# Optimization experiments

Measured on AMD Instinct MI355X. Metric: run time of the kernel, lower is better.

The kernel has to match this reference:

```python
import jax, jax.numpy as jnp
import numpy as np

EPS = 1e-5

def _layernorm(x, g, b):
    mu = jnp.mean(x, axis=-1, keepdims=True)
    var = jnp.mean(jnp.square(x - mu), axis=-1, keepdims=True)
    return (x - mu) * jax.lax.rsqrt(var + EPS) * g + b

def _mlp(x, w1, b1, w2, b2):
    h = jax.nn.gelu(jnp.einsum('bnd,dh->bnh', x, w1) + b1, approximate=False)
    return jnp.einsum('bnh,hd->bnd', h, w2) + b2

def setup_inputs() -> dict:
    key = jax.random.key(0)
    B, N, D, H = 2, 8192, 1024, 4096
    ks = jax.random.split(key, 12)
    s1 = 1.0 / np.sqrt(D)
    s2 = 1.0 / np.sqrt(H)
    return {
        'x': jax.random.normal(ks[0], (B, N, D), dtype=jnp.float32),
        'mask': jax.random.randint(ks[1], (B, N), 0, 2) > 0,
        'g_rgb': jnp.ones((D,), jnp.float32),
        'b_rgb': jnp.zeros((D,), jnp.float32),
        'w1_rgb': jax.random.normal(ks[2], (D, H), dtype=jnp.float32) * s1,
        'b1_rgb': jnp.zeros((H,), jnp.float32),
        'w2_rgb': jax.random.normal(ks[3], (H, D), dtype=jnp.float32) * s2,
        'b2_rgb': jnp.zeros((D,), jnp.float32),
        'g_expr': jnp.ones((D,), jnp.float32),
        'b_expr': jnp.zeros((D,), jnp.float32),
        'w1_expr': jax.random.normal(ks[4], (D, H), dtype=jnp.float32) * s1,
        'b1_expr': jnp.zeros((H,), jnp.float32),
        'w2_expr': jax.random.normal(ks[5], (H, D), dtype=jnp.float32) * s2,
        'b2_expr': jnp.zeros((D,), jnp.float32),
    }

def reference(x, mask, g_rgb, b_rgb, w1_rgb, b1_rgb, w2_rgb, b2_rgb,
              g_expr, b_expr, w1_expr, b1_expr, w2_expr, b2_expr):
    # Per-token routing: rgb expert where mask, expr expert where ~mask.
    # LayerNorm+MLP are pointwise per token, so dense compute + select is
    # mathematically identical to the torch gather->compute->scatter.
    z_rgb = _mlp(_layernorm(x, g_rgb, b_rgb), w1_rgb, b1_rgb, w2_rgb, b2_rgb)
    z_expr = _mlp(_layernorm(x, g_expr, b_expr), w1_expr, b1_expr, w2_expr, b2_expr)
    z = jnp.where(mask[..., None], z_rgb, z_expr)
    return z.astype(jnp.float16)  # torch scatters into a float16 buffer
```

## Files before the change

### kernel.cpp

```cpp
#include <hip/hip_runtime.h>
#include <hip/hip_bf16.h>
#include <hip/hip_fp16.h>

#define D_ 1024
#define H_ 4096
#define NTOK 16384
#define MPAD 16640

typedef __attribute__((ext_vector_type(8))) short bf16x8;
typedef __attribute__((ext_vector_type(4))) float f32x4;

static __device__ __forceinline__ unsigned short f2bf(float f) {
  union { float f; unsigned u; } x; x.f = f;
  unsigned u = x.u + 0x7fffu + ((x.u >> 16) & 1u);
  return (unsigned short)(u >> 16);
}

static __device__ __forceinline__ void gld16(const void* g, void* l) {
  __builtin_amdgcn_global_load_lds(
      (const __attribute__((address_space(1))) unsigned int*)g,
      (__attribute__((address_space(3))) unsigned int*)l, 16, 0, 0);
}

static __device__ __forceinline__ float gelu_fast(float x) {
  const float z = x * (1.5957691216f + 0.0713548163f * x * x);
  return x * __builtin_amdgcn_rcpf(1.0f + __expf(-z));
}

__global__ __launch_bounds__(256) void transpose4_kernel(
    const float* __restrict__ w1r, const float* __restrict__ w1e,
    const float* __restrict__ w2r, const float* __restrict__ w2e,
    unsigned short* __restrict__ o1r, unsigned short* __restrict__ o1e,
    unsigned short* __restrict__ o2r, unsigned short* __restrict__ o2e) {
  __shared__ float tile[64][65];
  const int t = blockIdx.x;
  const float* src; unsigned short* dst; int R, C, tl;
  if (t < 1024)       { src = w1r; dst = o1r; R = D_; C = H_; tl = t; }
  else if (t < 2048)  { src = w1e; dst = o1e; R = D_; C = H_; tl = t - 1024; }
  else if (t < 3072)  { src = w2r; dst = o2r; R = H_; C = D_; tl = t - 2048; }
  else                { src = w2e; dst = o2e; R = H_; C = D_; tl = t - 3072; }
  const int tc = C >> 6;
  const int r0 = (tl / tc) * 64, c0 = (tl % tc) * 64;
  const int tx = threadIdx.x & 63, ty = threadIdx.x >> 6;
#pragma unroll
  for (int i = 0; i < 64; i += 4)
    tile[ty + i][tx] = src[(size_t)(r0 + ty + i) * C + c0 + tx];
  __syncthreads();
  const int wl = threadIdx.x & 31, wrow = threadIdx.x >> 5;
#pragma unroll
  for (int i = 0; i < 64; i += 8) {
    const int orow = wrow + i;
    const unsigned lo = f2bf(tile[2 * wl][orow]);
    const unsigned hi = f2bf(tile[2 * wl + 1][orow]);
    *(unsigned*)(dst + (size_t)(c0 + orow) * R + r0 + 2 * wl) = lo | (hi << 16);
  }
}

__global__ __launch_bounds__(256) void compact_kernel(
    const int* __restrict__ mask, int* __restrict__ perm, int* __restrict__ counts) {
  const int NT = 256, CH = NTOK / NT;
  __shared__ int sm[NTOK];
  __shared__ int wsum[4];
  const int t = threadIdx.x;
  const int ln = t & 63, wv = t >> 6;
  for (int i = t; i < NTOK; i += NT) sm[i] = mask[i];
  for (int i = t; i < MPAD; i += NT) perm[i] = -1;
  __syncthreads();
  const int base = t * CH;
  int cnt = 0;
  for (int i = 0; i < CH; ++i) cnt += (sm[base + i] != 0);
  int sc = cnt;
#pragma unroll
  for (int o = 1; o < 64; o <<= 1) {
    int u = __shfl_up(sc, o, 64);
    if (ln >= o) sc += u;
  }
  if (ln == 63) wsum[wv] = sc;
  __syncthreads();
  int woff = 0;
#pragma unroll
  for (int j = 0; j < 4; ++j) woff += (j < wv) ? wsum[j] : 0;
  const int total1 = wsum[0] + wsum[1] + wsum[2] + wsum[3];
  if (t == 0) { counts[0] = total1; counts[1] = NTOK - total1; }
  const int excl = woff + sc - cnt;
  const int expr_base = ((total1 + 255) >> 8) << 8;
  int p1 = excl;
  int p0 = expr_base + (base - excl);
  for (int i = 0; i < CH; ++i) {
    const int idx = base + i;
    if (sm[idx] != 0) perm[p1++] = idx; else perm[p0++] = idx;
  }
}

__global__ __launch_bounds__(512) void ln_kernel(
    const float* __restrict__ x, const int* __restrict__ mask,
    const int* __restrict__ perm,
    const float* __restrict__ g_rgb, const float* __restrict__ b_rgb,
    const float* __restrict__ g_expr, const float* __restrict__ b_expr,
    unsigned short* __restrict__ xln) {
  const int h = threadIdx.x >> 8;
  const int tid = threadIdx.x & 255;
  const int i = blockIdx.x * 2 + h;
  int t = perm[i];
  const bool live = t >= 0;
  if (!live) t = 0;
  const float4 v = ((const float4*)(x + (size_t)t * D_))[tid];
  float s = v.x + v.y + v.z + v.w;
  float ss = v.x * v.x + v.y * v.y + v.z * v.z + v.w * v.w;
#pragma unroll
  for (int o = 32; o > 0; o >>= 1) {
    s += __shfl_xor(s, o, 64);
    ss += __shfl_xor(ss, o, 64);
  }
  __shared__ float red[16];
  const int wv = threadIdx.x >> 6, ln = threadIdx.x & 63;
  if (ln == 0) { red[wv] = s; red[8 + wv] = ss; }
  __syncthreads();
  const int rb = h * 4;
  s = red[rb + 0] + red[rb + 1] + red[rb + 2] + red[rb + 3];
  ss = red[8 + rb + 0] + red[8 + rb + 1] + red[8 + rb + 2] + red[8 + rb + 3];
  const float mu = s * (1.0f / D_);
  const float var = ss * (1.0f / D_) - mu * mu;
  const float rs = rsqrtf(var + 1e-5f);
  const bool rgb = mask[t] != 0;
  const float4 gv = ((const float4*)(rgb ? g_rgb : g_expr))[tid];
  const float4 bv = ((const float4*)(rgb ? b_rgb : b_expr))[tid];
  const unsigned short o0 = f2bf((v.x - mu) * rs * gv.x + bv.x);
  const unsigned short o1 = f2bf((v.y - mu) * rs * gv.y + bv.y);
  const unsigned short o2 = f2bf((v.z - mu) * rs * gv.z + bv.z);
  const unsigned short o3 = f2bf((v.w - mu) * rs * gv.w + bv.w);
  uint2 pk;
  pk.x = (unsigned)o0 | ((unsigned)o1 << 16);
  pk.y = (unsigned)o2 | ((unsigned)o3 << 16);
  if (live) *((uint2*)(xln + (size_t)i * D_ + tid * 4)) = pk;
}

template <int K, int N>
__global__ __launch_bounds__(512, 2) void gemm8_kernel(
    const unsigned short* __restrict__ A,
    const unsigned short* __restrict__ Wt_rgb,
    const unsigned short* __restrict__ Wt_expr,
    const float* __restrict__ bias_rgb,
    const float* __restrict__ bias_expr,
    const int* __restrict__ counts,
    unsigned short* __restrict__ Out) {
  constexpr int MT = MPAD / 256;
  constexpr int NT = N / 256;
  constexpr int ntk = K / 64;
  constexpr int KH2 = 128 * K * 2;

  const int tid = threadIdx.x;
  const int id = blockIdx.x;
  const int xcd = id & 7;
  const int slot = id >> 3;
  const int p = xcd * ((MT * NT) / 8) + slot;
  const int m0 = (p / NT) * 256;
  const int n0 = (p % NT) * 256;
  const int cnt_rgb = counts[0];
  const unsigned short* Wt = (m0 < cnt_rgb) ? Wt_rgb : Wt_expr;
  const float* bias = (m0 < cnt_rgb) ? bias_rgb : bias_expr;

  __shared__ unsigned short As[2][256 * 64];
  __shared__ unsigned short Bs[2][256 * 64];

  const int lane = tid & 63, wave = tid >> 6;
  const int wr = wave >> 2, wc = wave & 3;
  const int quad = lane >> 4, l16 = lane & 15;

  f32x4 acc[8][4] = {};

  const char* Abase = (const char*)A;
  const char* Wbase = (const char*)Wt;

  int agK0, agK1, bgK0, bgK1, sl0, sl1;
  {
    const int s0 = tid, s1 = 512 + tid;
    const int r0 = s0 >> 3, r1 = s1 >> 3;
    const int ks0 = ((s0 ^ r0) & 7) * 8, ks1 = ((s1 ^ r1) & 7) * 8;
    agK0 = ((m0 + r0) * K + ks0) * 2;  agK1 = ((m0 + r1) * K + ks1) * 2;
    bgK0 = ((n0 + r0) * K + ks0) * 2;  bgK1 = ((n0 + r1) * K + ks1) * 2;
    sl0 = s0 * 16;  sl1 = s1 * 16;
  }

  int aoffL[2][2][4];
  int boffL[2][4];
#pragma unroll
  for (int kk = 0; kk < 2; ++kk) {
    const int cb = kk * 4 + quad;
#pragma unroll
    for (int mh = 0; mh < 2; ++mh)
#pragma unroll
      for (int mi = 0; mi < 4; ++mi) {
        const int row = wr * 128 + mh * 64 + mi * 16 + l16;
        aoffL[kk][mh][mi] = (row * 64 + ((cb ^ row) & 7) * 8) * 2;
      }
#pragma unroll
    for (int ni = 0; ni < 4; ++ni) {
      const int row = wc * 64 + ni * 16 + l16;
      boffL[kk][ni] = (row * 64 + ((cb ^ row) & 7) * 8) * 2;
    }
  }

  bf16x8 a0, a1, a2, a3;
  bf16x8 bb[4];

#define STAGE_A(T1, HA, Q) do { \
    gld16(Abase + agK0 + (HA) * KH2 + (T1) * 128, (char*)As + (Q) * 32768 + (HA) * 16384 + sl0); \
    gld16(Abase + agK1 + (HA) * KH2 + (T1) * 128, (char*)As + (Q) * 32768 + (HA) * 16384 + sl1); \
  } while (0)
#define STAGE_B(T2, HB, Q) do { \
    gld16(Wbase + bgK0 + (HB) * KH2 + (T2) * 128, (char*)Bs + (Q) * 32768 + (HB) * 16384 + sl0); \
    gld16(Wbase + bgK1 + (HB) * KH2 + (T2) * 128, (char*)Bs + (Q) * 32768 + (HB) * 16384 + sl1); \
  } while (0)
#define RD_A(P_, KK, MH) do { \
    const char* _ab = (const char*)As + (P_) * 32768; \
    a0 = *(const bf16x8*)(_ab + aoffL[KK][MH][0]); \
    a1 = *(const bf16x8*)(_ab + aoffL[KK][MH][1]); \
    a2 = *(const bf16x8*)(_ab + aoffL[KK][MH][2]); \
    a3 = *(const bf16x8*)(_ab + aoffL[KK][MH][3]); \
  } while (0)
#define RD_B(P_, KK) do { \
    const char* _bp = (const char*)Bs + (P_) * 32768; \
    bb[0] = *(const bf16x8*)(_bp + boffL[KK][0]); \
    bb[1] = *(const bf16x8*)(_bp + boffL[KK][1]); \
    bb[2] = *(const bf16x8*)(_bp + boffL[KK][2]); \
    bb[3] = *(const bf16x8*)(_bp + boffL[KK][3]); \
  } while (0)
#define MFMA16(MO) do { \
    acc[(MO)+0][0] = __builtin_amdgcn_mfma_f32_16x16x32_bf16(a0, bb[0], acc[(MO)+0][0], 0, 0, 0); \
    acc[(MO)+0][1] = __builtin_amdgcn_mfma_f32_16x16x32_bf16(a0, bb[1], acc[(MO)+0][1], 0, 0, 0); \
    acc[(MO)+0][2] = __builtin_amdgcn_mfma_f32_16x16x32_bf16(a0, bb[2], acc[(MO)+0][2], 0, 0, 0); \
    acc[(MO)+0][3] = __builtin_amdgcn_mfma_f32_16x16x32_bf16(a0, bb[3], acc[(MO)+0][3], 0, 0, 0); \
    acc[(MO)+1][0] = __builtin_amdgcn_mfma_f32_16x16x32_bf16(a1, bb[0], acc[(MO)+1][0], 0, 0, 0); \
    acc[(MO)+1][1] = __builtin_amdgcn_mfma_f32_16x16x32_bf16(a1, bb[1], acc[(MO)+1][1], 0, 0, 0); \
    acc[(MO)+1][2] = __builtin_amdgcn_mfma_f32_16x16x32_bf16(a1, bb[2], acc[(MO)+1][2], 0, 0, 0); \
    acc[(MO)+1][3] = __builtin_amdgcn_mfma_f32_16x16x32_bf16(a1, bb[3], acc[(MO)+1][3], 0, 0, 0); \
    acc[(MO)+2][0] = __builtin_amdgcn_mfma_f32_16x16x32_bf16(a2, bb[0], acc[(MO)+2][0], 0, 0, 0); \
    acc[(MO)+2][1] = __builtin_amdgcn_mfma_f32_16x16x32_bf16(a2, bb[1], acc[(MO)+2][1], 0, 0, 0); \
    acc[(MO)+2][2] = __builtin_amdgcn_mfma_f32_16x16x32_bf16(a2, bb[2], acc[(MO)+2][2], 0, 0, 0); \
    acc[(MO)+2][3] = __builtin_amdgcn_mfma_f32_16x16x32_bf16(a2, bb[3], acc[(MO)+2][3], 0, 0, 0); \
    acc[(MO)+3][0] = __builtin_amdgcn_mfma_f32_16x16x32_bf16(a3, bb[0], acc[(MO)+3][0], 0, 0, 0); \
    acc[(MO)+3][1] = __builtin_amdgcn_mfma_f32_16x16x32_bf16(a3, bb[1], acc[(MO)+3][1], 0, 0, 0); \
    acc[(MO)+3][2] = __builtin_amdgcn_mfma_f32_16x16x32_bf16(a3, bb[2], acc[(MO)+3][2], 0, 0, 0); \
    acc[(MO)+3][3] = __builtin_amdgcn_mfma_f32_16x16x32_bf16(a3, bb[3], acc[(MO)+3][3], 0, 0, 0); \
  } while (0)

#define KTILE(T_, P_, SA_, SB_, VMC_) do { \
     \
    RD_B(P_, 0); RD_A(P_, 0, 0); \
    if (SA_) STAGE_A((T_) + 1, 0, (P_) ^ 1); \
    __builtin_amdgcn_s_barrier(); \
    __builtin_amdgcn_s_setprio(1); MFMA16(0); __builtin_amdgcn_s_setprio(0); \
    __builtin_amdgcn_s_barrier(); \
     \
    RD_A(P_, 0, 1); \
    if (SA_) STAGE_A((T_) + 1, 1, (P_) ^ 1); \
    __builtin_amdgcn_s_barrier(); \
    __builtin_amdgcn_s_setprio(1); MFMA16(4); __builtin_amdgcn_s_setprio(0); \
    __builtin_amdgcn_s_barrier(); \
     \
    RD_B(P_, 1); RD_A(P_, 1, 0); \
    __builtin_amdgcn_s_barrier(); \
    __builtin_amdgcn_s_setprio(1); MFMA16(0); __builtin_amdgcn_s_setprio(0); \
    __builtin_amdgcn_s_barrier(); \
     \
    RD_A(P_, 1, 1); \
    if (SB_) { STAGE_B((T_) + 2, 0, P_); STAGE_B((T_) + 2, 1, P_); } \
    __builtin_amdgcn_s_barrier(); \
    __builtin_amdgcn_s_setprio(1); MFMA16(4); __builtin_amdgcn_s_setprio(0); \
    if ((VMC_) == 4) { asm volatile("s_waitcnt vmcnt(4)" ::: "memory"); } \
    else if ((VMC_) == 0) { asm volatile("s_waitcnt vmcnt(0)" ::: "memory"); } \
    __builtin_amdgcn_sched_barrier(0); \
    __builtin_amdgcn_s_barrier(); \
  } while (0)

  STAGE_A(0, 0, 0); STAGE_A(0, 1, 0);
  STAGE_B(0, 0, 0); STAGE_B(0, 1, 0);
  STAGE_B(1, 0, 1); STAGE_B(1, 1, 1);
  asm volatile("s_waitcnt vmcnt(4)" ::: "memory");
  __builtin_amdgcn_sched_barrier(0);
  __builtin_amdgcn_s_barrier();

  for (int tt = 0; tt < ntk / 2 - 1; ++tt) {
    const int t0 = tt * 2;
    KTILE(t0, 0, 1, 1, 4);
    KTILE(t0 + 1, 1, 1, 1, 4);
  }
  KTILE(ntk - 2, 0, 1, 0, 0);
  KTILE(ntk - 1, 1, 0, 0, -1);

#undef KTILE
#undef MFMA16
#undef RD_B
#undef RD_A
#undef STAGE_B
#undef STAGE_A

  float bv[4];
#pragma unroll
  for (int ni = 0; ni < 4; ++ni) bv[ni] = bias[n0 + wc * 64 + ni * 16 + l16];
#pragma unroll
  for (int mi = 0; mi < 8; ++mi) {
#pragma unroll
    for (int r = 0; r < 4; ++r) {
      const int row = m0 + wr * 128 + mi * 16 + quad * 4 + r;
      unsigned short* orow = Out + (size_t)row * N + n0 + wc * 64 + l16;
#pragma unroll
      for (int ni = 0; ni < 4; ++ni)
        orow[ni * 16] = f2bf(gelu_fast(acc[mi][ni][r] + bv[ni]));
    }
  }
}

template <int EP, int K, int N>
__global__ __launch_bounds__(256) void gemm_kernel(
    const unsigned short* __restrict__ A,
    const unsigned short* __restrict__ Wt_rgb,
    const unsigned short* __restrict__ Wt_expr,
    const float* __restrict__ bias_rgb,
    const float* __restrict__ bias_expr,
    const int* __restrict__ counts,
    const int* __restrict__ perm,
    void* __restrict__ OutP) {
  constexpr int BM = 128, BN = 128, BK = 64;
  constexpr int MT = MPAD / BM;
  constexpr int NT = N / BN;
  const int tid = threadIdx.x;
  const int id = blockIdx.x;
  const int xcd = id & 7;
  const int slot = id >> 3;
  const int p = xcd * ((MT * NT) / 8) + slot;
  const int m0 = (p / NT) * BM;
  const int n0 = (p % NT) * BN;
  const int cnt_rgb = counts[0];
  const unsigned short* Wt = (m0 < cnt_rgb) ? Wt_rgb : Wt_expr;
  const float* bias = (m0 < cnt_rgb) ? bias_rgb : bias_expr;

  __shared__ unsigned short As[BM * BK];
  __shared__ unsigned short Bs[BN * BK];

  f32x4 acc[4][4] = {};

  const int lane = tid & 63, wave = tid >> 6;
  const int wm = (wave & 1) * 64, wn = (wave >> 1) * 64;
  const int quad = lane >> 4, l16 = lane & 15;

  const char* Abase = (const char*)A;
  const char* Wbase = (const char*)Wt;
  const char* AsB = (const char*)As;
  const char* BsB = (const char*)Bs;

  int ag[4], bg[4], sl[4];
#pragma unroll
  for (int it = 0; it < 4; ++it) {
    const int s = it * 256 + tid;
    const int row = s >> 3;
    const int ks = ((s ^ row) & 7) * 8;
    ag[it] = ((m0 + row) * K + ks) * 2;
    bg[it] = ((n0 + row) * K + ks) * 2;
    sl[it] = s * 16;
  }
  int aoff[2][4], boff[2][4];
#pragma unroll
  for (int hh = 0; hh < 2; ++hh) {
    const int cb = hh * 4 + quad;
#pragma unroll
    for (int mi = 0; mi < 4; ++mi) {
      const int row = wm + mi * 16 + l16;
      aoff[hh][mi] = (row * BK + (((cb ^ row) & 7) << 3)) * 2;
    }
#pragma unroll
    for (int ni = 0; ni < 4; ++ni) {
      const int row = wn + ni * 16 + l16;
      boff[hh][ni] = (row * BK + (((cb ^ row) & 7) << 3)) * 2;
    }
  }

  for (int k0 = 0; k0 < K; k0 += BK) {
#pragma unroll
    for (int it = 0; it < 4; ++it) {
      gld16(Abase + ag[it], (void*)(AsB + sl[it]));
      gld16(Wbase + bg[it], (void*)(BsB + sl[it]));
      ag[it] += BK * 2;
      bg[it] += BK * 2;
    }
    __syncthreads();
#pragma unroll
    for (int hh = 0; hh < 2; ++hh) {
      bf16x8 a[4], b[4];
#pragma unroll
      for (int mi = 0; mi < 4; ++mi) a[mi] = *(const bf16x8*)(AsB + aoff[hh][mi]);
#pragma unroll
      for (int ni = 0; ni < 4; ++ni) b[ni] = *(const bf16x8*)(BsB + boff[hh][ni]);
#pragma unroll
      for (int mi = 0; mi < 4; ++mi)
#pragma unroll
        for (int ni = 0; ni < 4; ++ni)
          acc[mi][ni] = __builtin_amdgcn_mfma_f32_16x16x32_bf16(a[mi], b[ni], acc[mi][ni], 0, 0, 0);
    }
    __syncthreads();
  }

  float bv[4];
#pragma unroll
  for (int ni = 0; ni < 4; ++ni) bv[ni] = bias[n0 + wn + ni * 16 + l16];

#pragma unroll
  for (int mi = 0; mi < 4; ++mi) {
#pragma unroll
    for (int r = 0; r < 4; ++r) {
      const int row = m0 + wm + mi * 16 + quad * 4 + r;
      if (EP == 0) {
        unsigned short* orow = (unsigned short*)OutP + (size_t)row * N + n0 + wn + l16;
#pragma unroll
        for (int ni = 0; ni < 4; ++ni) {
          orow[ni * 16] = f2bf(gelu_fast(acc[mi][ni][r] + bv[ni]));
        }
      } else {
        const int p2 = perm[row];
        if (p2 < 0) continue;
        float* orow = (float*)OutP + (size_t)p2 * N + n0 + wn + l16;
#pragma unroll
        for (int ni = 0; ni < 4; ++ni) {
          float v = acc[mi][ni][r] + bv[ni];
          orow[ni * 16] = __half2float(__float2half_rn(v));
        }
      }
    }
  }
}

extern "C" void kernel_launch(void* const* d_in, const int* in_sizes, int n_in,
                              void* d_out, int out_size, void* d_ws, size_t ws_size,
                              hipStream_t stream) {
  const float* x       = (const float*)d_in[0];
  const int*   mask    = (const int*)d_in[1];
  const float* g_rgb   = (const float*)d_in[2];
  const float* b_rgb   = (const float*)d_in[3];
  const float* w1_rgb  = (const float*)d_in[4];
  const float* b1_rgb  = (const float*)d_in[5];
  const float* w2_rgb  = (const float*)d_in[6];
  const float* b2_rgb  = (const float*)d_in[7];
  const float* g_expr  = (const float*)d_in[8];
  const float* b_expr  = (const float*)d_in[9];
  const float* w1_expr = (const float*)d_in[10];
  const float* b1_expr = (const float*)d_in[11];
  const float* w2_expr = (const float*)d_in[12];
  const float* b2_expr = (const float*)d_in[13];

  char* w = (char*)d_ws;
  int* counts               = (int*)(w + 0);
  int* perm                 = (int*)(w + 256);
  unsigned short* w1t_rgb   = (unsigned short*)(w + 66816);
  unsigned short* w1t_expr  = (unsigned short*)(w + 8455424);
  unsigned short* w2t_rgb   = (unsigned short*)(w + 16844032);
  unsigned short* w2t_expr  = (unsigned short*)(w + 25232640);
  unsigned short* xln       = (unsigned short*)(w + 33621248);
  unsigned short* h         = (unsigned short*)(w + 67699968);

  compact_kernel<<<1, 256, 0, stream>>>(mask, perm, counts);

  transpose4_kernel<<<4096, 256, 0, stream>>>(
      w1_rgb, w1_expr, w2_rgb, w2_expr, w1t_rgb, w1t_expr, w2t_rgb, w2t_expr);

  ln_kernel<<<MPAD / 2, 512, 0, stream>>>(x, mask, perm, g_rgb, b_rgb, g_expr, b_expr, xln);

  gemm8_kernel<D_, H_><<<dim3((MPAD / 256) * (H_ / 256)), 512, 0, stream>>>(
      xln, w1t_rgb, w1t_expr, b1_rgb, b1_expr, counts, h);

  gemm_kernel<1, H_, D_><<<dim3((D_ / 128) * (MPAD / 128)), 256, 0, stream>>>(
      h, w2t_rgb, w2t_expr, b2_rgb, b2_expr, counts, perm, d_out);
}
```

Before: 578.0 us.

## Fold mask compaction into transpose kernel and split second GEMM into halves

The single-block compaction kernel becomes an extra block of the weight transpose kernel, sharing LDS through a union. This removes one launch and lets the compaction run alongside the transpose blocks. The second GEMM is now launched twice over the two halves of the padded M range, with an mbase offset. The split adds one launch and changes how tiles are spread across XCDs, and the union enlarges every transpose block's LDS to about 64KB, which can lower that kernel's occupancy.

After: 591.3 us. +2.3%, slower.

```diff
diff --git a/kernel.cpp b/kernel.cpp
--- a/kernel.cpp
+++ b/kernel.cpp
@@ -31,9 +31,46 @@
     const float* __restrict__ w1r, const float* __restrict__ w1e,
     const float* __restrict__ w2r, const float* __restrict__ w2e,
     unsigned short* __restrict__ o1r, unsigned short* __restrict__ o1e,
-    unsigned short* __restrict__ o2r, unsigned short* __restrict__ o2e) {
-  __shared__ float tile[64][65];
+    unsigned short* __restrict__ o2r, unsigned short* __restrict__ o2e,
+    const int* __restrict__ mask, int* __restrict__ perm, int* __restrict__ counts) {
+  __shared__ union SMem {
+    float tile[64][65];
+    struct { int sm[NTOK]; int wsum[4]; } c;
+  } u;
   const int t = blockIdx.x;
+  if (t == 4096) {
+    const int NT = 256, CH = NTOK / NT;
+    const int tt = threadIdx.x;
+    const int ln = tt & 63, wv = tt >> 6;
+    for (int i = tt; i < NTOK; i += NT) u.c.sm[i] = mask[i];
+    for (int i = tt; i < MPAD; i += NT) perm[i] = -1;
+    __syncthreads();
+    const int base = tt * CH;
+    int cnt = 0;
+    for (int i = 0; i < CH; ++i) cnt += (u.c.sm[base + i] != 0);
+    int sc = cnt;
+#pragma unroll
+    for (int o = 1; o < 64; o <<= 1) {
+      int up = __shfl_up(sc, o, 64);
+      if (ln >= o) sc += up;
+    }
+    if (ln == 63) u.c.wsum[wv] = sc;
+    __syncthreads();
+    int woff = 0;
+#pragma unroll
+    for (int j = 0; j < 4; ++j) woff += (j < wv) ? u.c.wsum[j] : 0;
+    const int total1 = u.c.wsum[0] + u.c.wsum[1] + u.c.wsum[2] + u.c.wsum[3];
+    if (tt == 0) { counts[0] = total1; counts[1] = NTOK - total1; }
+    const int excl = woff + sc - cnt;
+    const int expr_base = ((total1 + 255) >> 8) << 8;
+    int p1 = excl;
+    int p0 = expr_base + (base - excl);
+    for (int i = 0; i < CH; ++i) {
+      const int idx = base + i;
+      if (u.c.sm[idx] != 0) perm[p1++] = idx; else perm[p0++] = idx;
+    }
+    return;
+  }
   const float* src; unsigned short* dst; int R, C, tl;
   if (t < 1024)       { src = w1r; dst = o1r; R = D_; C = H_; tl = t; }
   else if (t < 2048)  { src = w1e; dst = o1e; R = D_; C = H_; tl = t - 1024; }
@@ -44,51 +81,15 @@
   const int tx = threadIdx.x & 63, ty = threadIdx.x >> 6;
 #pragma unroll
   for (int i = 0; i < 64; i += 4)
-    tile[ty + i][tx] = src[(size_t)(r0 + ty + i) * C + c0 + tx];
+    u.tile[ty + i][tx] = src[(size_t)(r0 + ty + i) * C + c0 + tx];
   __syncthreads();
   const int wl = threadIdx.x & 31, wrow = threadIdx.x >> 5;
 #pragma unroll
   for (int i = 0; i < 64; i += 8) {
     const int orow = wrow + i;
-    const unsigned lo = f2bf(tile[2 * wl][orow]);
-    const unsigned hi = f2bf(tile[2 * wl + 1][orow]);
+    const unsigned lo = f2bf(u.tile[2 * wl][orow]);
+    const unsigned hi = f2bf(u.tile[2 * wl + 1][orow]);
     *(unsigned*)(dst + (size_t)(c0 + orow) * R + r0 + 2 * wl) = lo | (hi << 16);
-  }
-}
-
-__global__ __launch_bounds__(256) void compact_kernel(
-    const int* __restrict__ mask, int* __restrict__ perm, int* __restrict__ counts) {
-  const int NT = 256, CH = NTOK / NT;
-  __shared__ int sm[NTOK];
-  __shared__ int wsum[4];
-  const int t = threadIdx.x;
-  const int ln = t & 63, wv = t >> 6;
-  for (int i = t; i < NTOK; i += NT) sm[i] = mask[i];
-  for (int i = t; i < MPAD; i += NT) perm[i] = -1;
-  __syncthreads();
-  const int base = t * CH;
-  int cnt = 0;
-  for (int i = 0; i < CH; ++i) cnt += (sm[base + i] != 0);
-  int sc = cnt;
-#pragma unroll
-  for (int o = 1; o < 64; o <<= 1) {
-    int u = __shfl_up(sc, o, 64);
-    if (ln >= o) sc += u;
-  }
-  if (ln == 63) wsum[wv] = sc;
-  __syncthreads();
-  int woff = 0;
-#pragma unroll
-  for (int j = 0; j < 4; ++j) woff += (j < wv) ? wsum[j] : 0;
-  const int total1 = wsum[0] + wsum[1] + wsum[2] + wsum[3];
-  if (t == 0) { counts[0] = total1; counts[1] = NTOK - total1; }
-  const int excl = woff + sc - cnt;
-  const int expr_base = ((total1 + 255) >> 8) << 8;
-  int p1 = excl;
-  int p0 = expr_base + (base - excl);
-  for (int i = 0; i < CH; ++i) {
-    const int idx = base + i;
-    if (sm[idx] != 0) perm[p1++] = idx; else perm[p0++] = idx;
   }
 }
 
@@ -321,16 +322,17 @@
     const float* __restrict__ bias_expr,
     const int* __restrict__ counts,
     const int* __restrict__ perm,
-    void* __restrict__ OutP) {
+    void* __restrict__ OutP,
+    const int mbase) {
   constexpr int BM = 128, BN = 128, BK = 64;
-  constexpr int MT = MPAD / BM;
+  constexpr int MTH = (MPAD / 2) / BM;
   constexpr int NT = N / BN;
   const int tid = threadIdx.x;
   const int id = blockIdx.x;
   const int xcd = id & 7;
   const int slot = id >> 3;
-  const int p = xcd * ((MT * NT) / 8) + slot;
-  const int m0 = (p / NT) * BM;
+  const int p = xcd * ((MTH * NT) / 8) + slot;
+  const int m0 = mbase + (p / NT) * BM;
   const int n0 = (p % NT) * BN;
   const int cnt_rgb = counts[0];
   const unsigned short* Wt = (m0 < cnt_rgb) ? Wt_rgb : Wt_expr;
@@ -458,16 +460,17 @@
   unsigned short* xln       = (unsigned short*)(w + 33621248);
   unsigned short* h         = (unsigned short*)(w + 67699968);
 
-  compact_kernel<<<1, 256, 0, stream>>>(mask, perm, counts);
-
-  transpose4_kernel<<<4096, 256, 0, stream>>>(
-      w1_rgb, w1_expr, w2_rgb, w2_expr, w1t_rgb, w1t_expr, w2t_rgb, w2t_expr);
+  transpose4_kernel<<<4097, 256, 0, stream>>>(
+      w1_rgb, w1_expr, w2_rgb, w2_expr, w1t_rgb, w1t_expr, w2t_rgb, w2t_expr,
+      mask, perm, counts);
 
   ln_kernel<<<MPAD / 2, 512, 0, stream>>>(x, mask, perm, g_rgb, b_rgb, g_expr, b_expr, xln);
 
   gemm8_kernel<D_, H_><<<dim3((MPAD / 256) * (H_ / 256)), 512, 0, stream>>>(
       xln, w1t_rgb, w1t_expr, b1_rgb, b1_expr, counts, h);
 
-  gemm_kernel<1, H_, D_><<<dim3((D_ / 128) * (MPAD / 128)), 256, 0, stream>>>(
-      h, w2t_rgb, w2t_expr, b2_rgb, b2_expr, counts, perm, d_out);
-}
+  gemm_kernel<1, H_, D_><<<dim3((D_ / 128) * (MPAD / 2 / 128)), 256, 0, stream>>>(
+      h, w2t_rgb, w2t_expr, b2_rgb, b2_expr, counts, perm, d_out, 0);
+  gemm_kernel<1, H_, D_><<<dim3((D_ / 128) * (MPAD / 2 / 128)), 256, 0, stream>>>(
+      h, w2t_rgb, w2t_expr, b2_rgb, b2_expr, counts, perm, d_out, MPAD / 2);
+}
```
